# Optimization experiments

Hardware: AMD Instinct MI355X
Metric: run time of the kernel (lower is better)

## Reference

```python
import jax, jax.numpy as jnp
import numpy as np
from itertools import combinations

B, F, C, MAX_ORDER = 4096, 32, 128, 3


def setup_inputs() -> dict:
    key = jax.random.key(0)
    ks = jax.random.split(key, 1 + MAX_ORDER)
    x = jax.random.normal(ks[0], (B, F), dtype=jnp.float32)
    # Exact combinatorial index lists, matching get_index_lists (all k-subsets, lexicographic)
    idx = [jnp.asarray(np.array(list(combinations(range(F), o)), dtype=np.int32))
           for o in range(1, MAX_ORDER + 1)]
    # Per-order Dense kernels [n_combos, num_classes] (glorot-ish scale), no bias (use_bias=False)
    Ws = [jax.random.normal(ks[i + 1], (idx[i].shape[0], C), dtype=jnp.float32)
          * (2.0 / (idx[i].shape[0] + C)) ** 0.5 for i in range(MAX_ORDER)]
    bias = jnp.zeros((1, C), dtype=jnp.float32)  # Zeros initializer
    return {"x": x, "bias": bias,
            "W1": Ws[0], "W2": Ws[1], "W3": Ws[2],
            "idx1": idx[0], "idx2": idx[1], "idx3": idx[2]}


def reference(x, bias, W1, W2, W3, idx1, idx2, idx3):
    # combine(): out = tile(bias) + sum_i Dense_i( prod over feature-subset of order i )
    out = jnp.broadcast_to(bias, (x.shape[0], bias.shape[1]))
    for idx, W in ((idx1, W1), (idx2, W2), (idx3, W3)):
        # x[:, idx]: [B, n_combos, order] gather; product over subset axis -> [B, n_combos]
        prods = jnp.prod(x[:, idx], axis=2)
        out = out + prods @ W  # [B, num_classes]
    return out
```

## Files before the change

kernel.cpp:

```cpp
#include <hip/hip_runtime.h>
#include <hip/hip_bf16.h>
#include <hip/hip_fp16.h>

constexpr int B_   = 4096;
constexpr int C_   = 128;
constexpr int K1   = 32;
constexpr int K2   = 496;
constexpr int K3   = 4960;
constexpr int KTOT = K1 + K2 + K3;
constexpr int KPAD = 5632;

constexpr int SPLITK = 16;
constexpr int KSEG   = KPAD / SPLITK;
constexpr int CHUNKS = KSEG / 16;
constexpr int BM     = 64;

typedef __attribute__((ext_vector_type(8)))  short bf16x8;
typedef __attribute__((ext_vector_type(16))) float f32x16;

constexpr size_t WS_WT   = 0;
constexpr size_t WS_PART = 1572864;

struct Sched { short a[KPAD]; short b[KPAD]; short c[KPAD]; };
constexpr Sched make_sched() {
    Sched s{}; int k = 0;
    for (int i = 0; i < 32; ++i) { s.a[k] = i; s.b[k] = 32; s.c[k] = 32; ++k; }
    for (int i = 0; i < 32; ++i)
        for (int j = i + 1; j < 32; ++j) { s.a[k] = i; s.b[k] = j; s.c[k] = 32; ++k; }
    for (int i = 0; i < 32; ++i)
        for (int j = i + 1; j < 32; ++j)
            for (int l = j + 1; l < 32; ++l) { s.a[k] = i; s.b[k] = j; s.c[k] = l; ++k; }
    for (; k < KPAD; ++k) { s.a[k] = 32; s.b[k] = 32; s.c[k] = 32; }
    return s;
}
constexpr Sched SCH = make_sched();

template<int K>
__device__ __forceinline__ float prodK(const float (&xv)[33]) {
    return xv[SCH.a[K]] * xv[SCH.b[K]] * xv[SCH.c[K]];
}

template<int K0, int J>
__device__ __forceinline__ void prods8(const float (&xv)[33], bool hi, float (&q)[8]) {
    if constexpr (J < 8) {
        q[J] = hi ? prodK<K0 + 8 + J>(xv) : prodK<K0 + J>(xv);
        prods8<K0, J + 1>(xv, hi, q);
    }
}

template<int SEG, int CH>
__device__ __forceinline__ void run_chunks(const float (&xv)[33], bool hi, int lane, int ct0,
                                           const ushort* __restrict__ Wb,
                                           f32x16& acc0, f32x16& acc1) {
    if constexpr (CH < CHUNKS) {
        constexpr int K0 = SEG * KSEG + CH * 16;
        constexpr int G  = SEG * CHUNKS + CH;
        const ushort* wp = Wb + ((size_t)(G * 4 + ct0) * 64 + lane) * 8;
        bf16x8 b0 = *(const bf16x8*)wp;
        bf16x8 b1 = *(const bf16x8*)(wp + 64 * 8);
        float q[8];
        prods8<K0, 0>(xv, hi, q);
        union { ushort us[8]; bf16x8 v; } af;
        #pragma unroll
        for (int j = 0; j < 8; ++j) {
            __hip_bfloat16 h = __float2bfloat16(q[j]);
            af.us[j] = *reinterpret_cast<ushort*>(&h);
        }
        acc0 = __builtin_amdgcn_mfma_f32_32x32x16_bf16(af.v, b0, acc0, 0, 0, 0);
        acc1 = __builtin_amdgcn_mfma_f32_32x32x16_bf16(af.v, b1, acc1, 0, 0, 0);
        run_chunks<SEG, CH + 1>(xv, hi, lane, ct0, Wb, acc0, acc1);
    }
}

__global__ __launch_bounds__(256)
void prep_wt(const float* __restrict__ W1,
             const float* __restrict__ W2,
             const float* __restrict__ W3,
             ushort* __restrict__ Wb)
{
    __shared__ ushort tile[16 * 130];
    const int gc = blockIdx.x, t = threadIdx.x;
    const int k0 = gc * 16;
    #pragma unroll
    for (int p = 0; p < 2; ++p) {
        int e  = p * 256 + t;
        int kk = e >> 5, cq = e & 31;
        int k  = k0 + kk;
        float4 v = {0.f, 0.f, 0.f, 0.f};
        if (k < K1)           v = ((const float4*)W1)[k * 32 + cq];
        else if (k < K1 + K2) v = ((const float4*)W2)[(k - K1) * 32 + cq];
        else if (k < KTOT)    v = ((const float4*)W3)[(k - K1 - K2) * 32 + cq];
        union { ushort u[4]; uint2 d; } o;
        __hip_bfloat16 h0 = __float2bfloat16(v.x); o.u[0] = *(ushort*)&h0;
        __hip_bfloat16 h1 = __float2bfloat16(v.y); o.u[1] = *(ushort*)&h1;
        __hip_bfloat16 h2 = __float2bfloat16(v.z); o.u[2] = *(ushort*)&h2;
        __hip_bfloat16 h3 = __float2bfloat16(v.w); o.u[3] = *(ushort*)&h3;
        *(uint2*)&tile[kk * 130 + cq * 4] = o.d;
    }
    __syncthreads();
    {
        int ct = t >> 6, lane = t & 63, n = lane & 31, kg = lane >> 5;
        union { ushort us[8]; uint4 d; } o;
        #pragma unroll
        for (int j = 0; j < 8; ++j) o.us[j] = tile[(kg * 8 + j) * 130 + ct * 32 + n];
        *(uint4*)&Wb[((size_t)(gc * 4 + ct) * 64 + lane) * 8] = o.d;
    }
}

__global__ __launch_bounds__(256, 4)
void poly_mfma(const float* __restrict__ x,
               const ushort* __restrict__ Wb,
               __half* __restrict__ part)
{
    __shared__ ushort epi[BM * 132];

    const int t    = threadIdx.x;
    const int lane = t & 63;
    const int w    = t >> 6;
    const int rt   = w >> 1;
    const int ct0  = (w & 1) * 2;
    const int m    = lane & 31;
    const bool hi  = lane >= 32;
    const int row0 = blockIdx.x * BM;

    float xv[33];
    {
        const float4* xrow = (const float4*)(x + (size_t)(row0 + rt * 32 + m) * 32);
        #pragma unroll
        for (int qv = 0; qv < 8; ++qv) {
            float4 v = xrow[qv];
            xv[qv * 4 + 0] = v.x; xv[qv * 4 + 1] = v.y;
            xv[qv * 4 + 2] = v.z; xv[qv * 4 + 3] = v.w;
        }
        xv[32] = 1.0f;
    }

    f32x16 acc0, acc1;
    #pragma unroll
    for (int i = 0; i < 16; ++i) { acc0[i] = 0.f; acc1[i] = 0.f; }

    switch (blockIdx.y) {
        case 0:  run_chunks<0, 0>(xv, hi, lane, ct0, Wb, acc0, acc1); break;
        case 1:  run_chunks<1, 0>(xv, hi, lane, ct0, Wb, acc0, acc1); break;
        case 2:  run_chunks<2, 0>(xv, hi, lane, ct0, Wb, acc0, acc1); break;
        case 3:  run_chunks<3, 0>(xv, hi, lane, ct0, Wb, acc0, acc1); break;
        case 4:  run_chunks<4, 0>(xv, hi, lane, ct0, Wb, acc0, acc1); break;
        case 5:  run_chunks<5, 0>(xv, hi, lane, ct0, Wb, acc0, acc1); break;
        case 6:  run_chunks<6, 0>(xv, hi, lane, ct0, Wb, acc0, acc1); break;
        case 7:  run_chunks<7, 0>(xv, hi, lane, ct0, Wb, acc0, acc1); break;
        case 8:  run_chunks<8, 0>(xv, hi, lane, ct0, Wb, acc0, acc1); break;
        case 9:  run_chunks<9, 0>(xv, hi, lane, ct0, Wb, acc0, acc1); break;
        case 10: run_chunks<10, 0>(xv, hi, lane, ct0, Wb, acc0, acc1); break;
        case 11: run_chunks<11, 0>(xv, hi, lane, ct0, Wb, acc0, acc1); break;
        case 12: run_chunks<12, 0>(xv, hi, lane, ct0, Wb, acc0, acc1); break;
        case 13: run_chunks<13, 0>(xv, hi, lane, ct0, Wb, acc0, acc1); break;
        case 14: run_chunks<14, 0>(xv, hi, lane, ct0, Wb, acc0, acc1); break;
        default: run_chunks<15, 0>(xv, hi, lane, ct0, Wb, acc0, acc1); break;
    }

    const int kg = hi ? 1 : 0;
    #pragma unroll
    for (int cti = 0; cti < 2; ++cti) {
        int col = (ct0 + cti) * 32 + m;
        #pragma unroll
        for (int e = 0; e < 16; ++e) {
            int r = rt * 32 + (e & 3) + 8 * (e >> 2) + 4 * kg;
            float v = cti ? acc1[e] : acc0[e];
            __half h = __float2half(v);
            epi[r * 132 + col] = *reinterpret_cast<ushort*>(&h);
        }
    }
    __syncthreads();
    {
        const size_t pbase = (size_t)blockIdx.y * (B_ * C_) + (size_t)row0 * C_;
        #pragma unroll
        for (int p = 0; p < 4; ++p) {
            int Gg = p * 256 + t;
            int r = Gg >> 4, g = Gg & 15;
            uint4 v;
            v.x = *(const uint*)&epi[r * 132 + g * 8];
            v.y = *(const uint*)&epi[r * 132 + g * 8 + 2];
            v.z = *(const uint*)&epi[r * 132 + g * 8 + 4];
            v.w = *(const uint*)&epi[r * 132 + g * 8 + 6];
            *(uint4*)((ushort*)part + pbase + r * C_ + g * 8) = v;
        }
    }
}

__global__ __launch_bounds__(256)
void reduce_k(const __half* __restrict__ part,
              const float* __restrict__ bias,
              float* __restrict__ out)
{
    int i = (blockIdx.x * 256 + threadIdx.x) * 8;
    const float4* bp = (const float4*)&bias[i & (C_ - 1)];
    float4 b0 = bp[0], b1 = bp[1];
    float s[8] = {b0.x, b0.y, b0.z, b0.w, b1.x, b1.y, b1.z, b1.w};
    #pragma unroll
    for (int sp = 0; sp < SPLITK; ++sp) {
        uint4 v = *(const uint4*)&part[(size_t)sp * (B_ * C_) + i];
        const __half2* h2 = (const __half2*)&v;
        #pragma unroll
        for (int j = 0; j < 4; ++j) {
            float2 f = __half22float2(h2[j]);
            s[2*j] += f.x; s[2*j+1] += f.y;
        }
    }
    float4 o0 = {s[0], s[1], s[2], s[3]};
    float4 o1 = {s[4], s[5], s[6], s[7]};
    *(float4*)&out[i]     = o0;
    *(float4*)&out[i + 4] = o1;
}

extern "C" void kernel_launch(void* const* d_in, const int* in_sizes, int n_in,
                              void* d_out, int out_size, void* d_ws, size_t ws_size,
                              hipStream_t stream)
{
    const float* x    = (const float*)d_in[0];
    const float* bias = (const float*)d_in[1];
    const float* W1   = (const float*)d_in[2];
    const float* W2   = (const float*)d_in[3];
    const float* W3   = (const float*)d_in[4];
    float* out = (float*)d_out;

    ushort* Wb    = (ushort*)((char*)d_ws + WS_WT);
    __half* partp = (__half*)((char*)d_ws + WS_PART);

    prep_wt<<<KPAD / 16, 256, 0, stream>>>(W1, W2, W3, Wb);

    dim3 grid(B_ / BM, SPLITK);
    poly_mfma<<<grid, 256, 0, stream>>>(x, Wb, partp);

    reduce_k<<<(B_ * C_) / 8 / 256, 256, 0, stream>>>(partp, bias, out);
}
```

Before: 96.36 us.

## Fuse split-K reduction into GEMM kernel via last-block atomic counter

Removes the separate reduce kernel launch. Each split-K block bumps a per-row-block atomic counter after writing its fp16 partials, and the last block to arrive sums all 16 partials plus the bias and writes the output. The counters are zeroed in the weight-prep kernel. This saves one launch and lets the reduction overlap with other blocks' work, at the cost of a threadfence and atomic per block and a serial tail reduction done by a single block.

After: 204.8 us. 2.13x slower.

```diff
diff --git a/kernel.cpp b/kernel.cpp
--- a/kernel.cpp
+++ b/kernel.cpp
@@ -20,6 +20,7 @@
 
 constexpr size_t WS_WT   = 0;
 constexpr size_t WS_PART = 1572864;
+constexpr size_t WS_CNT  = 18350080;
 
 struct Sched { short a[KPAD]; short b[KPAD]; short c[KPAD]; };
 constexpr Sched make_sched() {
@@ -76,10 +77,12 @@
 void prep_wt(const float* __restrict__ W1,
              const float* __restrict__ W2,
              const float* __restrict__ W3,
-             ushort* __restrict__ Wb)
+             ushort* __restrict__ Wb,
+             uint* __restrict__ cnt)
 {
     __shared__ ushort tile[16 * 130];
     const int gc = blockIdx.x, t = threadIdx.x;
+    if (gc == 0 && t < 64) cnt[t] = 0;
     const int k0 = gc * 16;
     #pragma unroll
     for (int p = 0; p < 2; ++p) {
@@ -110,9 +113,13 @@
 __global__ __launch_bounds__(256, 4)
 void poly_mfma(const float* __restrict__ x,
                const ushort* __restrict__ Wb,
-               __half* __restrict__ part)
+               __half* __restrict__ part,
+               const float* __restrict__ bias,
+               float* __restrict__ out,
+               uint* __restrict__ cnt)
 {
     __shared__ ushort epi[BM * 132];
+    __shared__ int lastFlag;
 
     const int t    = threadIdx.x;
     const int lane = t & 63;
@@ -121,7 +128,8 @@
     const int ct0  = (w & 1) * 2;
     const int m    = lane & 31;
     const bool hi  = lane >= 32;
-    const int row0 = blockIdx.x * BM;
+    const int rb   = blockIdx.x;
+    const int row0 = rb * BM;
 
     float xv[33];
     {
@@ -185,31 +193,39 @@
             *(uint4*)((ushort*)part + pbase + r * C_ + g * 8) = v;
         }
     }
-}
-
-__global__ __launch_bounds__(256)
-void reduce_k(const __half* __restrict__ part,
-              const float* __restrict__ bias,
-              float* __restrict__ out)
-{
-    int i = (blockIdx.x * 256 + threadIdx.x) * 8;
-    const float4* bp = (const float4*)&bias[i & (C_ - 1)];
-    float4 b0 = bp[0], b1 = bp[1];
-    float s[8] = {b0.x, b0.y, b0.z, b0.w, b1.x, b1.y, b1.z, b1.w};
-    #pragma unroll
-    for (int sp = 0; sp < SPLITK; ++sp) {
-        uint4 v = *(const uint4*)&part[(size_t)sp * (B_ * C_) + i];
-        const __half2* h2 = (const __half2*)&v;
-        #pragma unroll
-        for (int j = 0; j < 4; ++j) {
-            float2 f = __half22float2(h2[j]);
-            s[2*j] += f.x; s[2*j+1] += f.y;
-        }
-    }
-    float4 o0 = {s[0], s[1], s[2], s[3]};
-    float4 o1 = {s[4], s[5], s[6], s[7]};
-    *(float4*)&out[i]     = o0;
-    *(float4*)&out[i + 4] = o1;
+
+    __threadfence();
+    __syncthreads();
+    if (t == 0) {
+        uint old = atomicAdd(&cnt[rb], 1u);
+        lastFlag = (old == SPLITK - 1);
+    }
+    __syncthreads();
+    if (lastFlag) {
+        __threadfence();
+        const size_t rbase = (size_t)rb * (BM * C_);
+        #pragma unroll
+        for (int p = 0; p < 4; ++p) {
+            int i = p * 2048 + t * 8;
+            const float4* bp = (const float4*)&bias[i & (C_ - 1)];
+            float4 b0 = bp[0], b1 = bp[1];
+            float s[8] = {b0.x, b0.y, b0.z, b0.w, b1.x, b1.y, b1.z, b1.w};
+            #pragma unroll
+            for (int sp = 0; sp < SPLITK; ++sp) {
+                uint4 v = *(const uint4*)&part[(size_t)sp * (B_ * C_) + rbase + i];
+                const __half2* h2 = (const __half2*)&v;
+                #pragma unroll
+                for (int j = 0; j < 4; ++j) {
+                    float2 f = __half22float2(h2[j]);
+                    s[2*j] += f.x; s[2*j+1] += f.y;
+                }
+            }
+            float4 o0 = {s[0], s[1], s[2], s[3]};
+            float4 o1 = {s[4], s[5], s[6], s[7]};
+            *(float4*)&out[rbase + i]     = o0;
+            *(float4*)&out[rbase + i + 4] = o1;
+        }
+    }
 }
 
 extern "C" void kernel_launch(void* const* d_in, const int* in_sizes, int n_in,
@@ -225,11 +241,10 @@
 
     ushort* Wb    = (ushort*)((char*)d_ws + WS_WT);
     __half* partp = (__half*)((char*)d_ws + WS_PART);
-
-    prep_wt<<<KPAD / 16, 256, 0, stream>>>(W1, W2, W3, Wb);
+    uint*   cnt   = (uint*)((char*)d_ws + WS_CNT);
+
+    prep_wt<<<KPAD / 16, 256, 0, stream>>>(W1, W2, W3, Wb, cnt);
 
     dim3 grid(B_ / BM, SPLITK);
-    poly_mfma<<<grid, 256, 0, stream>>>(x, Wb, partp);
-
-    reduce_k<<<(B_ * C_) / 8 / 256, 256, 0, stream>>>(partp, bias, out);
-}
+    poly_mfma<<<grid, 256, 0, stream>>>(x, Wb, partp, bias, out, cnt);
+}
```

## Replace global split-K partials with in-block wave split-K and fused LDS reduction

Applied to the files above, without the earlier changes.

Each block now covers 32 rows by one 32-column tile. Its four waves each take a quarter of K and are reduced in shared memory, with the bias added in the same epilogue. This removes the fp16 partial buffer written to global memory and the separate reduce kernel launch. In exchange, each wave recomputes the triple products for its column tile, so product arithmetic per MFMA roughly doubles (one MFMA per chunk instead of two). The full 5632-deep K loop is also fully unrolled in each wave, and occupancy is lowered to two blocks per CU.

Result: faster. 82.31 us, median of 2 (-14.6%).

```diff
diff --git a/kernel.cpp b/kernel.cpp
--- a/kernel.cpp
+++ b/kernel.cpp
@@ -1,6 +1,5 @@
 #include <hip/hip_runtime.h>
 #include <hip/hip_bf16.h>
-#include <hip/hip_fp16.h>
 
 constexpr int B_   = 4096;
 constexpr int C_   = 128;
@@ -10,16 +9,13 @@
 constexpr int KTOT = K1 + K2 + K3;
 constexpr int KPAD = 5632;
 
-constexpr int SPLITK = 16;
-constexpr int KSEG   = KPAD / SPLITK;
-constexpr int CHUNKS = KSEG / 16;
-constexpr int BM     = 64;
+constexpr int NCHUNK = KPAD / 16;
+constexpr int WCH    = NCHUNK / 4;
 
 typedef __attribute__((ext_vector_type(8)))  short bf16x8;
 typedef __attribute__((ext_vector_type(16))) float f32x16;
 
-constexpr size_t WS_WT   = 0;
-constexpr size_t WS_PART = 1572864;
+constexpr size_t WS_WT = 0;
 
 struct Sched { short a[KPAD]; short b[KPAD]; short c[KPAD]; };
 constexpr Sched make_sched() {
@@ -48,16 +44,13 @@
     }
 }
 
-template<int SEG, int CH>
-__device__ __forceinline__ void run_chunks(const float (&xv)[33], bool hi, int lane, int ct0,
-                                           const ushort* __restrict__ Wb,
-                                           f32x16& acc0, f32x16& acc1) {
-    if constexpr (CH < CHUNKS) {
-        constexpr int K0 = SEG * KSEG + CH * 16;
-        constexpr int G  = SEG * CHUNKS + CH;
-        const ushort* wp = Wb + ((size_t)(G * 4 + ct0) * 64 + lane) * 8;
-        bf16x8 b0 = *(const bf16x8*)wp;
-        bf16x8 b1 = *(const bf16x8*)(wp + 64 * 8);
+template<int WV, int CH>
+__device__ __forceinline__ void run_chunks(const float (&xv)[33], bool hi, int lane, int ct,
+                                           const ushort* __restrict__ Wb, f32x16& acc) {
+    if constexpr (CH < WCH) {
+        constexpr int G  = WV * WCH + CH;
+        constexpr int K0 = G * 16;
+        bf16x8 b0 = *(const bf16x8*)(Wb + ((size_t)(G * 4 + ct) * 64 + lane) * 8);
         float q[8];
         prods8<K0, 0>(xv, hi, q);
         union { ushort us[8]; bf16x8 v; } af;
@@ -66,9 +59,8 @@
             __hip_bfloat16 h = __float2bfloat16(q[j]);
             af.us[j] = *reinterpret_cast<ushort*>(&h);
         }
-        acc0 = __builtin_amdgcn_mfma_f32_32x32x16_bf16(af.v, b0, acc0, 0, 0, 0);
-        acc1 = __builtin_amdgcn_mfma_f32_32x32x16_bf16(af.v, b1, acc1, 0, 0, 0);
-        run_chunks<SEG, CH + 1>(xv, hi, lane, ct0, Wb, acc0, acc1);
+        acc = __builtin_amdgcn_mfma_f32_32x32x16_bf16(af.v, b0, acc, 0, 0, 0);
+        run_chunks<WV, CH + 1>(xv, hi, lane, ct, Wb, acc);
     }
 }
 
@@ -107,25 +99,25 @@
     }
 }
 
-__global__ __launch_bounds__(256, 4)
+__global__ __launch_bounds__(256, 2)
 void poly_mfma(const float* __restrict__ x,
                const ushort* __restrict__ Wb,
-               __half* __restrict__ part)
+               const float* __restrict__ bias,
+               float* __restrict__ out)
 {
-    __shared__ ushort epi[BM * 132];
+    __shared__ float red[4][32 * 33];
 
     const int t    = threadIdx.x;
     const int lane = t & 63;
     const int w    = t >> 6;
-    const int rt   = w >> 1;
-    const int ct0  = (w & 1) * 2;
     const int m    = lane & 31;
     const bool hi  = lane >= 32;
-    const int row0 = blockIdx.x * BM;
+    const int row0 = blockIdx.x * 32;
+    const int ct   = blockIdx.y;
 
     float xv[33];
     {
-        const float4* xrow = (const float4*)(x + (size_t)(row0 + rt * 32 + m) * 32);
+        const float4* xrow = (const float4*)(x + (size_t)(row0 + m) * 32);
         #pragma unroll
         for (int qv = 0; qv < 8; ++qv) {
             float4 v = xrow[qv];
@@ -135,81 +127,38 @@
         xv[32] = 1.0f;
     }
 
-    f32x16 acc0, acc1;
+    f32x16 acc;
     #pragma unroll
-    for (int i = 0; i < 16; ++i) { acc0[i] = 0.f; acc1[i] = 0.f; }
+    for (int i = 0; i < 16; ++i) acc[i] = 0.f;
 
-    switch (blockIdx.y) {
-        case 0:  run_chunks<0, 0>(xv, hi, lane, ct0, Wb, acc0, acc1); break;
-        case 1:  run_chunks<1, 0>(xv, hi, lane, ct0, Wb, acc0, acc1); break;
-        case 2:  run_chunks<2, 0>(xv, hi, lane, ct0, Wb, acc0, acc1); break;
-        case 3:  run_chunks<3, 0>(xv, hi, lane, ct0, Wb, acc0, acc1); break;
-        case 4:  run_chunks<4, 0>(xv, hi, lane, ct0, Wb, acc0, acc1); break;
-        case 5:  run_chunks<5, 0>(xv, hi, lane, ct0, Wb, acc0, acc1); break;
-        case 6:  run_chunks<6, 0>(xv, hi, lane, ct0, Wb, acc0, acc1); break;
-        case 7:  run_chunks<7, 0>(xv, hi, lane, ct0, Wb, acc0, acc1); break;
-        case 8:  run_chunks<8, 0>(xv, hi, lane, ct0, Wb, acc0, acc1); break;
-        case 9:  run_chunks<9, 0>(xv, hi, lane, ct0, Wb, acc0, acc1); break;
-        case 10: run_chunks<10, 0>(xv, hi, lane, ct0, Wb, acc0, acc1); break;
-        case 11: run_chunks<11, 0>(xv, hi, lane, ct0, Wb, acc0, acc1); break;
-        case 12: run_chunks<12, 0>(xv, hi, lane, ct0, Wb, acc0, acc1); break;
-        case 13: run_chunks<13, 0>(xv, hi, lane, ct0, Wb, acc0, acc1); break;
-        case 14: run_chunks<14, 0>(xv, hi, lane, ct0, Wb, acc0, acc1); break;
-        default: run_chunks<15, 0>(xv, hi, lane, ct0, Wb, acc0, acc1); break;
+    switch (w) {
+        case 0:  run_chunks<0, 0>(xv, hi, lane, ct, Wb, acc); break;
+        case 1:  run_chunks<1, 0>(xv, hi, lane, ct, Wb, acc); break;
+        case 2:  run_chunks<2, 0>(xv, hi, lane, ct, Wb, acc); break;
+        default: run_chunks<3, 0>(xv, hi, lane, ct, Wb, acc); break;
     }
 
     const int kg = hi ? 1 : 0;
     #pragma unroll
-    for (int cti = 0; cti < 2; ++cti) {
-        int col = (ct0 + cti) * 32 + m;
-        #pragma unroll
-        for (int e = 0; e < 16; ++e) {
-            int r = rt * 32 + (e & 3) + 8 * (e >> 2) + 4 * kg;
-            float v = cti ? acc1[e] : acc0[e];
-            __half h = __float2half(v);
-            epi[r * 132 + col] = *reinterpret_cast<ushort*>(&h);
-        }
+    for (int e = 0; e < 16; ++e) {
+        int r = (e & 3) + 8 * (e >> 2) + 4 * kg;
+        red[w][r * 33 + m] = acc[e];
     }
     __syncthreads();
+
     {
-        const size_t pbase = (size_t)blockIdx.y * (B_ * C_) + (size_t)row0 * C_;
+        int r  = t >> 3;
+        int c0 = (t & 7) * 4;
+        float4 b = *(const float4*)&bias[ct * 32 + c0];
+        float s[4] = {b.x, b.y, b.z, b.w};
         #pragma unroll
-        for (int p = 0; p < 4; ++p) {
-            int Gg = p * 256 + t;
-            int r = Gg >> 4, g = Gg & 15;
-            uint4 v;
-            v.x = *(const uint*)&epi[r * 132 + g * 8];
-            v.y = *(const uint*)&epi[r * 132 + g * 8 + 2];
-            v.z = *(const uint*)&epi[r * 132 + g * 8 + 4];
-            v.w = *(const uint*)&epi[r * 132 + g * 8 + 6];
-            *(uint4*)((ushort*)part + pbase + r * C_ + g * 8) = v;
-        }
+        for (int wv = 0; wv < 4; ++wv)
+            #pragma unroll
+            for (int j = 0; j < 4; ++j)
+                s[j] += red[wv][r * 33 + c0 + j];
+        float4 o = {s[0], s[1], s[2], s[3]};
+        *(float4*)&out[(size_t)(row0 + r) * C_ + ct * 32 + c0] = o;
     }
-}
-
-__global__ __launch_bounds__(256)
-void reduce_k(const __half* __restrict__ part,
-              const float* __restrict__ bias,
-              float* __restrict__ out)
-{
-    int i = (blockIdx.x * 256 + threadIdx.x) * 8;
-    const float4* bp = (const float4*)&bias[i & (C_ - 1)];
-    float4 b0 = bp[0], b1 = bp[1];
-    float s[8] = {b0.x, b0.y, b0.z, b0.w, b1.x, b1.y, b1.z, b1.w};
-    #pragma unroll
-    for (int sp = 0; sp < SPLITK; ++sp) {
-        uint4 v = *(const uint4*)&part[(size_t)sp * (B_ * C_) + i];
-        const __half2* h2 = (const __half2*)&v;
-        #pragma unroll
-        for (int j = 0; j < 4; ++j) {
-            float2 f = __half22float2(h2[j]);
-            s[2*j] += f.x; s[2*j+1] += f.y;
-        }
-    }
-    float4 o0 = {s[0], s[1], s[2], s[3]};
-    float4 o1 = {s[4], s[5], s[6], s[7]};
-    *(float4*)&out[i]     = o0;
-    *(float4*)&out[i + 4] = o1;
 }
 
 extern "C" void kernel_launch(void* const* d_in, const int* in_sizes, int n_in,
@@ -223,13 +172,10 @@
     const float* W3   = (const float*)d_in[4];
     float* out = (float*)d_out;
 
-    ushort* Wb    = (ushort*)((char*)d_ws + WS_WT);
-    __half* partp = (__half*)((char*)d_ws + WS_PART);
+    ushort* Wb = (ushort*)((char*)d_ws + WS_WT);
 
     prep_wt<<<KPAD / 16, 256, 0, stream>>>(W1, W2, W3, Wb);
 
-    dim3 grid(B_ / BM, SPLITK);
-    poly_mfma<<<grid, 256, 0, stream>>>(x, Wb, partp);
-
-    reduce_k<<<(B_ * C_) / 8 / 256, 256, 0, stream>>>(partp, bias, out);
+    dim3 grid(B_ / 32, C_ / 32);
+    poly_mfma<<<grid, 256, 0, stream>>>(x, Wb, bias, out);
 }
```
